# Optimization experiments

Measured on AMD Instinct MI355X. Metric: run time of the kernel, lower is better.

## Reference

```python
import jax, jax.numpy as jnp
import numpy as np

N_NODES = 50000
N_EDGES = 800000
IN_CH, HID_CH, OUT_CH = 128, 128, 64


def setup_inputs() -> dict:
    key = jax.random.key(0)
    k1, k2, k3, k4 = jax.random.split(key, 4)
    x = jax.random.normal(k1, (N_NODES, IN_CH), dtype=jnp.float32)
    edge_index = jax.random.randint(k2, (2, N_EDGES), 0, N_NODES, dtype=jnp.int64)
    W1 = jax.random.normal(k3, (IN_CH, HID_CH), dtype=jnp.float32) * (1.0 / np.sqrt(IN_CH))
    b1 = jnp.zeros((HID_CH,), dtype=jnp.float32)
    W2 = jax.random.normal(k4, (HID_CH, OUT_CH), dtype=jnp.float32) * (1.0 / np.sqrt(HID_CH))
    b2 = jnp.zeros((OUT_CH,), dtype=jnp.float32)
    return {"x": x, "edge_index": edge_index, "W1": W1, "b1": b1, "W2": W2, "b2": b2}


def _gcn_conv(x, src, dst, norm, W, b, n_nodes):
    # x' = D^-1/2 (A+I) D^-1/2 (x W) + b
    h = x @ W                                        # [N, C_out]
    msg = norm[:, None] * h[src]                     # gather + scale, [E', C_out]
    agg = jax.ops.segment_sum(msg, dst, num_segments=n_nodes)
    return agg + b


def reference(x, edge_index, W1, b1, W2, b2):
    n = x.shape[0]
    # add self loops
    loops = jnp.arange(n, dtype=edge_index.dtype)
    src = jnp.concatenate([edge_index[0], loops])
    dst = jnp.concatenate([edge_index[1], loops])
    # symmetric degree normalization computed on target index
    deg = jax.ops.segment_sum(jnp.ones_like(dst, dtype=x.dtype), dst, num_segments=n)
    dinv = jnp.where(deg > 0, jax.lax.rsqrt(deg), 0.0)
    norm = dinv[src] * dinv[dst]                     # [E']

    h = jax.nn.relu(_gcn_conv(x, src, dst, norm, W1, b1, n))
    logits = _gcn_conv(h, src, dst, norm, W2, b2, n)
    return jax.nn.softmax(logits, axis=1)
```

## Files before the change

kernel.cpp:

```cpp
#include <hip/hip_runtime.h>
#include <hip/hip_fp16.h>


#define SLOT 64
#define NB   49
#define CAP  18432
#define EPB  4096

__global__ __launch_bounds__(256) void k_part(const int* __restrict__ ei,
                                              int* __restrict__ bcur,
                                              unsigned int* __restrict__ bkt,
                                              int e) {
    __shared__ int sSrc[EPB];
    __shared__ int sDst[EPB];
    __shared__ int sCnt[64];
    int b0 = blockIdx.x * EPB;
    int cnt = min(EPB, e - b0);
    for (int i = threadIdx.x; i < cnt; i += 256) {
        sSrc[i] = ei[b0 + i];
        sDst[i] = ei[e + b0 + i];
    }
    if (threadIdx.x < 64) sCnt[threadIdx.x] = 0;
    __syncthreads();
    for (int i = threadIdx.x; i < cnt; i += 256)
        atomicAdd(&sCnt[sDst[i] >> 10], 1);
    __syncthreads();
    if (threadIdx.x < 64) {
        int c = sCnt[threadIdx.x];
        int gbase = (c > 0 && threadIdx.x < NB) ? atomicAdd(&bcur[threadIdx.x], c) : 0;
        sCnt[threadIdx.x] = gbase;
    }
    __syncthreads();
    for (int i = threadIdx.x; i < cnt; i += 256) {
        int d = sDst[i];
        int b = d >> 10;
        int pos = atomicAdd(&sCnt[b], 1);
        if (pos < CAP)
            bkt[(size_t)b * CAP + pos] =
                ((unsigned int)(d & 1023) << 16) | (unsigned int)sSrc[i];
    }
}

__global__ __launch_bounds__(256) void k_build(const int* __restrict__ bcur,
                                               const unsigned int* __restrict__ bkt,
                                               unsigned short* __restrict__ csr,
                                               int* __restrict__ deg,
                                               float* __restrict__ dinv, int n) {
    __shared__ unsigned short rows[256 * SLOT];
    __shared__ int cur[256];
    int r = blockIdx.x;
    int b = r >> 2;
    int q = r & 3;
    cur[threadIdx.x] = 0;
    __syncthreads();
    int cnt = min(bcur[b], CAP);
    const unsigned int* bp = bkt + (size_t)b * CAP;
    for (int i = threadIdx.x; i < cnt; i += 256) {
        unsigned int p = bp[i];
        int dl = (int)(p >> 16);
        if ((dl >> 8) == q) {
            int node = dl & 255;
            int pos = atomicAdd(&cur[node], 1);
            if (pos < SLOT) rows[node * SLOT + pos] = (unsigned short)(p & 0xffff);
        }
    }
    __syncthreads();
    int base = r * 256;
    uint4* dst4 = (uint4*)(csr + (size_t)base * SLOT);
    const uint4* src4 = (const uint4*)rows;
    for (int i = threadIdx.x; i < 256 * SLOT / 8; i += 256) dst4[i] = src4[i];
    int node = base + threadIdx.x;
    if (node < n) {
        int c = cur[threadIdx.x];
        deg[node] = c;
        dinv[node] = rsqrtf((float)(c + 1));
    }
}

__global__ __launch_bounds__(256, 4) void k_gemm1(
    const float* __restrict__ X, const float* __restrict__ W,
    __half* __restrict__ H, int n)
{
    __shared__ float sX[64 * 132];
    const int tid = threadIdx.x;
    const int r0 = blockIdx.x * 64;

    for (int i = tid; i < 64 * 32; i += 256) {
        int r = i >> 5, c4 = i & 31;
        float4 v = make_float4(0.f, 0.f, 0.f, 0.f);
        int gr = r0 + r;
        if (gr < n) v = ((const float4*)X)[(size_t)gr * 32 + c4];
        *(float4*)&sX[r * 132 + c4 * 4] = v;
    }
    __syncthreads();

    const int rg = tid >> 4;
    const int cg = tid & 15;
    float acc[4][8];
#pragma unroll
    for (int i = 0; i < 4; ++i)
#pragma unroll
        for (int j = 0; j < 8; ++j) acc[i][j] = 0.f;

    const float* sXr = sX + rg * 4 * 132;
    const float* Wc = W + cg * 8;
#pragma unroll 4
    for (int k = 0; k < 128; ++k) {
        float4 w0 = *(const float4*)(Wc + k * 128);
        float4 w1 = *(const float4*)(Wc + k * 128 + 4);
        float a[4];
#pragma unroll
        for (int i = 0; i < 4; ++i) a[i] = sXr[i * 132 + k];
        float w[8] = {w0.x, w0.y, w0.z, w0.w, w1.x, w1.y, w1.z, w1.w};
#pragma unroll
        for (int i = 0; i < 4; ++i)
#pragma unroll
            for (int j = 0; j < 8; ++j) acc[i][j] = fmaf(a[i], w[j], acc[i][j]);
    }

#pragma unroll
    for (int i = 0; i < 4; ++i) {
        int r = r0 + rg * 4 + i;
        if (r < n) {
            __half2 hp[4];
#pragma unroll
            for (int j = 0; j < 4; ++j)
                hp[j] = __floats2half2_rn(acc[i][2 * j], acc[i][2 * j + 1]);
            *(float4*)(H + (size_t)r * 128 + cg * 8) = *(float4*)hp;
        }
    }
}

__global__ __launch_bounds__(256) void k_agg1(
    const int* __restrict__ deg, const unsigned short* __restrict__ csr,
    const float* __restrict__ dinv, const __half* __restrict__ H,
    const float* __restrict__ b1, float* __restrict__ H1, int n)
{
    int node = blockIdx.x * 4 + (threadIdx.x >> 6);
    if (node >= n) return;
    int lane = threadIdx.x & 63;
    int g = lane >> 4, sub = lane & 15;
    float dd = dinv[node];

    float acc[8];
#pragma unroll
    for (int i = 0; i < 8; ++i) acc[i] = 0.f;

    int beg = node * SLOT;
    int cnt = min(deg[node], SLOT);
    {
        int m = cnt;
        int   s_l = (lane < m) ? (int)csr[beg + lane] : 0;
        float w_l = (lane < m) ? dinv[s_l] * dd : 0.f;
        int iters = (m + 3) >> 2;
#pragma unroll 4
        for (int t = 0; t < iters; ++t) {
            int j = 4 * t + g;
            int   s = __shfl(s_l, j);
            float w = __shfl(w_l, j);
            float4 raw = ((const float4*)(H + (size_t)s * 128))[sub];
            const __half2* h2 = (const __half2*)&raw;
#pragma unroll
            for (int q = 0; q < 4; ++q) {
                float2 v = __half22float2(h2[q]);
                acc[2 * q]     = fmaf(w, v.x, acc[2 * q]);
                acc[2 * q + 1] = fmaf(w, v.y, acc[2 * q + 1]);
            }
        }
    }
#pragma unroll
    for (int i = 0; i < 8; ++i) {
        acc[i] += __shfl_xor(acc[i], 16);
        acc[i] += __shfl_xor(acc[i], 32);
    }
    float4 sraw = ((const float4*)(H + (size_t)node * 128))[sub];
    const __half2* sh2 = (const __half2*)&sraw;
    float sl = dd * dd;
    float4 bb0 = ((const float4*)(b1 + sub * 8))[0];
    float4 bb1 = ((const float4*)(b1 + sub * 8))[1];
    float out[8];
#pragma unroll
    for (int q = 0; q < 4; ++q) {
        float2 v = __half22float2(sh2[q]);
        out[2 * q]     = fmaf(sl, v.x, acc[2 * q]);
        out[2 * q + 1] = fmaf(sl, v.y, acc[2 * q + 1]);
    }
    out[0] += bb0.x; out[1] += bb0.y; out[2] += bb0.z; out[3] += bb0.w;
    out[4] += bb1.x; out[5] += bb1.y; out[6] += bb1.z; out[7] += bb1.w;
#pragma unroll
    for (int i = 0; i < 8; ++i) out[i] = fmaxf(out[i], 0.f);
    float* op = H1 + (size_t)node * 128 + sub * 8;
    if (g == 0) *(float4*)op       = make_float4(out[0], out[1], out[2], out[3]);
    if (g == 1) *(float4*)(op + 4) = make_float4(out[4], out[5], out[6], out[7]);
}

__global__ __launch_bounds__(256, 4) void k_gemm2(
    const float* __restrict__ X, const float* __restrict__ W,
    __half* __restrict__ H2, int n)
{
    __shared__ float sX[64 * 132];
    const int tid = threadIdx.x;
    const int r0 = blockIdx.x * 64;

    for (int i = tid; i < 64 * 32; i += 256) {
        int r = i >> 5, c4 = i & 31;
        float4 v = make_float4(0.f, 0.f, 0.f, 0.f);
        int gr = r0 + r;
        if (gr < n) v = ((const float4*)X)[(size_t)gr * 32 + c4];
        *(float4*)&sX[r * 132 + c4 * 4] = v;
    }
    __syncthreads();

    const int rg = tid >> 4;
    const int cg = tid & 15;
    float acc[4][4];
#pragma unroll
    for (int i = 0; i < 4; ++i)
#pragma unroll
        for (int j = 0; j < 4; ++j) acc[i][j] = 0.f;

    const float* sXr = sX + rg * 4 * 132;
    const float* Wc = W + cg * 4;
#pragma unroll 4
    for (int k = 0; k < 128; ++k) {
        float4 w0 = *(const float4*)(Wc + k * 64);
        float a[4];
#pragma unroll
        for (int i = 0; i < 4; ++i) a[i] = sXr[i * 132 + k];
        float w[4] = {w0.x, w0.y, w0.z, w0.w};
#pragma unroll
        for (int i = 0; i < 4; ++i)
#pragma unroll
            for (int j = 0; j < 4; ++j) acc[i][j] = fmaf(a[i], w[j], acc[i][j]);
    }

#pragma unroll
    for (int i = 0; i < 4; ++i) {
        int r = r0 + rg * 4 + i;
        if (r < n) {
            __half2 hp[2];
            hp[0] = __floats2half2_rn(acc[i][0], acc[i][1]);
            hp[1] = __floats2half2_rn(acc[i][2], acc[i][3]);
            *(float2*)(H2 + (size_t)r * 64 + cg * 4) = *(float2*)hp;
        }
    }
}

__global__ __launch_bounds__(256) void k_agg2(
    const int* __restrict__ deg, const unsigned short* __restrict__ csr,
    const float* __restrict__ dinv, const __half* __restrict__ H2,
    const float* __restrict__ b2, float* __restrict__ OUT, int n)
{
    int node = blockIdx.x * 4 + (threadIdx.x >> 6);
    if (node >= n) return;
    int lane = threadIdx.x & 63;
    int g = lane >> 3, sub = lane & 7;
    float dd = dinv[node];

    float acc[8];
#pragma unroll
    for (int i = 0; i < 8; ++i) acc[i] = 0.f;

    int beg = node * SLOT;
    int cnt = min(deg[node], SLOT);
    {
        int m = cnt;
        int   s_l = (lane < m) ? (int)csr[beg + lane] : 0;
        float w_l = (lane < m) ? dinv[s_l] * dd : 0.f;
        int iters = (m + 7) >> 3;
#pragma unroll 4
        for (int t = 0; t < iters; ++t) {
            int j = 8 * t + g;
            int   s = __shfl(s_l, j);
            float w = __shfl(w_l, j);
            float4 raw = ((const float4*)(H2 + (size_t)s * 64))[sub];
            const __half2* h2 = (const __half2*)&raw;
#pragma unroll
            for (int q = 0; q < 4; ++q) {
                float2 v = __half22float2(h2[q]);
                acc[2 * q]     = fmaf(w, v.x, acc[2 * q]);
                acc[2 * q + 1] = fmaf(w, v.y, acc[2 * q + 1]);
            }
        }
    }
#pragma unroll
    for (int i = 0; i < 8; ++i) {
        acc[i] += __shfl_xor(acc[i], 8);
        acc[i] += __shfl_xor(acc[i], 16);
        acc[i] += __shfl_xor(acc[i], 32);
    }
    float4 sraw = ((const float4*)(H2 + (size_t)node * 64))[sub];
    const __half2* sh2 = (const __half2*)&sraw;
    float sl = dd * dd;
    float4 bb0 = ((const float4*)(b2 + sub * 8))[0];
    float4 bb1 = ((const float4*)(b2 + sub * 8))[1];
    float out[8];
#pragma unroll
    for (int q = 0; q < 4; ++q) {
        float2 v = __half22float2(sh2[q]);
        out[2 * q]     = fmaf(sl, v.x, acc[2 * q]);
        out[2 * q + 1] = fmaf(sl, v.y, acc[2 * q + 1]);
    }
    out[0] += bb0.x; out[1] += bb0.y; out[2] += bb0.z; out[3] += bb0.w;
    out[4] += bb1.x; out[5] += bb1.y; out[6] += bb1.z; out[7] += bb1.w;
    float mx = out[0];
#pragma unroll
    for (int i = 1; i < 8; ++i) mx = fmaxf(mx, out[i]);
    mx = fmaxf(mx, __shfl_xor(mx, 1));
    mx = fmaxf(mx, __shfl_xor(mx, 2));
    mx = fmaxf(mx, __shfl_xor(mx, 4));
    float sm = 0.f;
#pragma unroll
    for (int i = 0; i < 8; ++i) { out[i] = expf(out[i] - mx); sm += out[i]; }
    sm += __shfl_xor(sm, 1);
    sm += __shfl_xor(sm, 2);
    sm += __shfl_xor(sm, 4);
    float inv = 1.f / sm;
#pragma unroll
    for (int i = 0; i < 8; ++i) out[i] *= inv;
    float* op = OUT + (size_t)node * 64 + sub * 8;
    if (g == 0) *(float4*)op       = make_float4(out[0], out[1], out[2], out[3]);
    if (g == 1) *(float4*)(op + 4) = make_float4(out[4], out[5], out[6], out[7]);
}

extern "C" void kernel_launch(void* const* d_in, const int* in_sizes, int n_in,
                              void* d_out, int out_size, void* d_ws, size_t ws_size,
                              hipStream_t stream) {
    const float* X  = (const float*)d_in[0];
    const int*   EI = (const int*)d_in[1];
    const float* W1 = (const float*)d_in[2];
    const float* B1 = (const float*)d_in[3];
    const float* W2 = (const float*)d_in[4];
    const float* B2 = (const float*)d_in[5];
    float* OUT = (float*)d_out;

    const int n = in_sizes[0] / 128;
    const int e = in_sizes[1] / 2;

    const int np = (n + 255) & ~255;
    int*            bcur = (int*)d_ws;
    int*            deg  = bcur + 64;
    float*          dinv = (float*)(deg + np);
    unsigned int*   bkt  = (unsigned int*)(dinv + np);
    unsigned short* csr  = (unsigned short*)(bkt + (size_t)NB * CAP);
    __half*         H16  = (__half*)(csr + (size_t)np * SLOT);
    float*          H1   = (float*)(H16 + (size_t)np * 128);
    __half*         H2   = (__half*)(H1 + (size_t)n * 128);

    hipMemsetAsync(bcur, 0, 64 * sizeof(int), stream);
    k_part<<<(e + EPB - 1) / EPB, 256, 0, stream>>>(EI, bcur, bkt, e);
    k_build<<<np / 256, 256, 0, stream>>>(bcur, bkt, csr, deg, dinv, n);

    k_gemm1<<<(n + 63) / 64, 256, 0, stream>>>(X, W1, H16, n);
    k_agg1<<<(n + 3) / 4, 256, 0, stream>>>(deg, csr, dinv, H16, B1, H1, n);

    k_gemm2<<<(n + 63) / 64, 256, 0, stream>>>(H1, W2, H2, n);
    k_agg2<<<(n + 3) / 4, 256, 0, stream>>>(deg, csr, dinv, H2, B2, OUT, n);
}
```

Measured before the change: 241.4 us.

## Replace FP32 FMA GEMMs with split-fp16 MFMA matrix-core GEMMs

Both dense projections now run on MFMA 16x16x16 fp16 instructions instead of scalar FP32 FMAs through LDS. Each operand is split into hi and lo fp16 parts, and three MFMAs per tile keep accuracy close to FP32. A new kernel prepacks W1 and W2 into an MFMA-friendly split layout in the workspace. X is read straight from global memory with no shared-memory staging. The costs are one extra small launch and three MFMAs per tile, and the split-fp16 scheme can lose range for values outside fp16 limits.

```diff
diff --git a/kernel.cpp b/kernel.cpp
--- a/kernel.cpp
+++ b/kernel.cpp
@@ -6,6 +6,10 @@
 #define NB   49
 #define CAP  18432
 #define EPB  4096
+
+typedef _Float16 h4 __attribute__((ext_vector_type(4)));
+typedef _Float16 h8 __attribute__((ext_vector_type(8)));
+typedef float f4 __attribute__((ext_vector_type(4)));
 
 __global__ __launch_bounds__(256) void k_part(const int* __restrict__ ei,
                                               int* __restrict__ bcur,
@@ -77,56 +81,67 @@
     }
 }
 
-__global__ __launch_bounds__(256, 4) void k_gemm1(
-    const float* __restrict__ X, const float* __restrict__ W,
+__global__ __launch_bounds__(256) void k_splitw(const float* __restrict__ W1,
+                                                const float* __restrict__ W2,
+                                                _Float16* __restrict__ W1p,
+                                                _Float16* __restrict__ W2p) {
+    int i = blockIdx.x * 256 + threadIdx.x;
+    float w; int k, c; _Float16* dst;
+    if (i < 16384)      { k = i >> 7, c = i & 127; w = W1[i]; dst = W1p; }
+    else if (i < 24576) { int t = i - 16384; k = t >> 6; c = t & 63; w = W2[t]; dst = W2p; }
+    else return;
+    _Float16 hi = (_Float16)w;
+    _Float16 lo = (_Float16)(w - (float)hi);
+    int kc = k >> 4, kk = k & 15;
+    int l = (kk >> 2) * 16 + (c & 15);
+    int j = kk & 3;
+    int ct = c >> 4;
+    size_t base = ((size_t)(ct * 8 + kc) * 64 + l) * 8 + j;
+    dst[base] = hi;
+    dst[base + 4] = lo;
+}
+
+__global__ __launch_bounds__(256) void k_gemm1(
+    const float* __restrict__ X, const _Float16* __restrict__ Wp,
     __half* __restrict__ H, int n)
 {
-    __shared__ float sX[64 * 132];
-    const int tid = threadIdx.x;
-    const int r0 = blockIdx.x * 64;
-
-    for (int i = tid; i < 64 * 32; i += 256) {
-        int r = i >> 5, c4 = i & 31;
-        float4 v = make_float4(0.f, 0.f, 0.f, 0.f);
-        int gr = r0 + r;
-        if (gr < n) v = ((const float4*)X)[(size_t)gr * 32 + c4];
-        *(float4*)&sX[r * 132 + c4 * 4] = v;
-    }
-    __syncthreads();
-
-    const int rg = tid >> 4;
-    const int cg = tid & 15;
-    float acc[4][8];
-#pragma unroll
-    for (int i = 0; i < 4; ++i)
-#pragma unroll
-        for (int j = 0; j < 8; ++j) acc[i][j] = 0.f;
-
-    const float* sXr = sX + rg * 4 * 132;
-    const float* Wc = W + cg * 8;
-#pragma unroll 4
-    for (int k = 0; k < 128; ++k) {
-        float4 w0 = *(const float4*)(Wc + k * 128);
-        float4 w1 = *(const float4*)(Wc + k * 128 + 4);
-        float a[4];
-#pragma unroll
-        for (int i = 0; i < 4; ++i) a[i] = sXr[i * 132 + k];
-        float w[8] = {w0.x, w0.y, w0.z, w0.w, w1.x, w1.y, w1.z, w1.w};
-#pragma unroll
-        for (int i = 0; i < 4; ++i)
-#pragma unroll
-            for (int j = 0; j < 8; ++j) acc[i][j] = fmaf(a[i], w[j], acc[i][j]);
-    }
-
-#pragma unroll
-    for (int i = 0; i < 4; ++i) {
-        int r = r0 + rg * 4 + i;
-        if (r < n) {
-            __half2 hp[4];
-#pragma unroll
-            for (int j = 0; j < 4; ++j)
-                hp[j] = __floats2half2_rn(acc[i][2 * j], acc[i][2 * j + 1]);
-            *(float4*)(H + (size_t)r * 128 + cg * 8) = *(float4*)hp;
+    int w = threadIdx.x >> 6, lane = threadIdx.x & 63;
+    int r0 = blockIdx.x * 64 + w * 16;
+    int xr = r0 + (lane & 15);
+    int xrc = min(xr, n - 1);
+    const float* xp = X + (size_t)xrc * 128 + ((lane >> 4) * 4);
+
+    f4 acc[8];
+#pragma unroll
+    for (int ct = 0; ct < 8; ++ct) acc[ct] = (f4){0.f, 0.f, 0.f, 0.f};
+
+#pragma unroll
+    for (int kc = 0; kc < 8; ++kc) {
+        float4 xv = *(const float4*)(xp + kc * 16);
+        h4 xh, xl;
+        xh[0] = (_Float16)xv.x; xh[1] = (_Float16)xv.y;
+        xh[2] = (_Float16)xv.z; xh[3] = (_Float16)xv.w;
+        xl[0] = (_Float16)(xv.x - (float)xh[0]);
+        xl[1] = (_Float16)(xv.y - (float)xh[1]);
+        xl[2] = (_Float16)(xv.z - (float)xh[2]);
+        xl[3] = (_Float16)(xv.w - (float)xh[3]);
+#pragma unroll
+        for (int ct = 0; ct < 8; ++ct) {
+            h8 wb = ((const h8*)Wp)[(ct * 8 + kc) * 64 + lane];
+            h4 wh = {wb[0], wb[1], wb[2], wb[3]};
+            h4 wl = {wb[4], wb[5], wb[6], wb[7]};
+            acc[ct] = __builtin_amdgcn_mfma_f32_16x16x16f16(wh, xh, acc[ct], 0, 0, 0);
+            acc[ct] = __builtin_amdgcn_mfma_f32_16x16x16f16(wl, xh, acc[ct], 0, 0, 0);
+            acc[ct] = __builtin_amdgcn_mfma_f32_16x16x16f16(wh, xl, acc[ct], 0, 0, 0);
+        }
+    }
+    if (xr < n) {
+        __half* hp = H + (size_t)xr * 128 + (lane >> 4) * 4;
+#pragma unroll
+        for (int ct = 0; ct < 8; ++ct) {
+            h4 o = {(_Float16)acc[ct][0], (_Float16)acc[ct][1],
+                    (_Float16)acc[ct][2], (_Float16)acc[ct][3]};
+            *(h4*)(hp + ct * 16) = o;
         }
     }
 }
@@ -194,54 +209,47 @@
     if (g == 1) *(float4*)(op + 4) = make_float4(out[4], out[5], out[6], out[7]);
 }
 
-__global__ __launch_bounds__(256, 4) void k_gemm2(
-    const float* __restrict__ X, const float* __restrict__ W,
+__global__ __launch_bounds__(256) void k_gemm2(
+    const float* __restrict__ X, const _Float16* __restrict__ Wp,
     __half* __restrict__ H2, int n)
 {
-    __shared__ float sX[64 * 132];
-    const int tid = threadIdx.x;
-    const int r0 = blockIdx.x * 64;
-
-    for (int i = tid; i < 64 * 32; i += 256) {
-        int r = i >> 5, c4 = i & 31;
-        float4 v = make_float4(0.f, 0.f, 0.f, 0.f);
-        int gr = r0 + r;
-        if (gr < n) v = ((const float4*)X)[(size_t)gr * 32 + c4];
-        *(float4*)&sX[r * 132 + c4 * 4] = v;
-    }
-    __syncthreads();
-
-    const int rg = tid >> 4;
-    const int cg = tid & 15;
-    float acc[4][4];
-#pragma unroll
-    for (int i = 0; i < 4; ++i)
-#pragma unroll
-        for (int j = 0; j < 4; ++j) acc[i][j] = 0.f;
-
-    const float* sXr = sX + rg * 4 * 132;
-    const float* Wc = W + cg * 4;
-#pragma unroll 4
-    for (int k = 0; k < 128; ++k) {
-        float4 w0 = *(const float4*)(Wc + k * 64);
-        float a[4];
-#pragma unroll
-        for (int i = 0; i < 4; ++i) a[i] = sXr[i * 132 + k];
-        float w[4] = {w0.x, w0.y, w0.z, w0.w};
-#pragma unroll
-        for (int i = 0; i < 4; ++i)
-#pragma unroll
-            for (int j = 0; j < 4; ++j) acc[i][j] = fmaf(a[i], w[j], acc[i][j]);
-    }
-
-#pragma unroll
-    for (int i = 0; i < 4; ++i) {
-        int r = r0 + rg * 4 + i;
-        if (r < n) {
-            __half2 hp[2];
-            hp[0] = __floats2half2_rn(acc[i][0], acc[i][1]);
-            hp[1] = __floats2half2_rn(acc[i][2], acc[i][3]);
-            *(float2*)(H2 + (size_t)r * 64 + cg * 4) = *(float2*)hp;
+    int w = threadIdx.x >> 6, lane = threadIdx.x & 63;
+    int r0 = blockIdx.x * 64 + w * 16;
+    int xr = r0 + (lane & 15);
+    int xrc = min(xr, n - 1);
+    const float* xp = X + (size_t)xrc * 128 + ((lane >> 4) * 4);
+
+    f4 acc[4];
+#pragma unroll
+    for (int ct = 0; ct < 4; ++ct) acc[ct] = (f4){0.f, 0.f, 0.f, 0.f};
+
+#pragma unroll
+    for (int kc = 0; kc < 8; ++kc) {
+        float4 xv = *(const float4*)(xp + kc * 16);
+        h4 xh, xl;
+        xh[0] = (_Float16)xv.x; xh[1] = (_Float16)xv.y;
+        xh[2] = (_Float16)xv.z; xh[3] = (_Float16)xv.w;
+        xl[0] = (_Float16)(xv.x - (float)xh[0]);
+        xl[1] = (_Float16)(xv.y - (float)xh[1]);
+        xl[2] = (_Float16)(xv.z - (float)xh[2]);
+        xl[3] = (_Float16)(xv.w - (float)xh[3]);
+#pragma unroll
+        for (int ct = 0; ct < 4; ++ct) {
+            h8 wb = ((const h8*)Wp)[(ct * 8 + kc) * 64 + lane];
+            h4 wh = {wb[0], wb[1], wb[2], wb[3]};
+            h4 wl = {wb[4], wb[5], wb[6], wb[7]};
+            acc[ct] = __builtin_amdgcn_mfma_f32_16x16x16f16(wh, xh, acc[ct], 0, 0, 0);
+            acc[ct] = __builtin_amdgcn_mfma_f32_16x16x16f16(wl, xh, acc[ct], 0, 0, 0);
+            acc[ct] = __builtin_amdgcn_mfma_f32_16x16x16f16(wh, xl, acc[ct], 0, 0, 0);
+        }
+    }
+    if (xr < n) {
+        __half* hp = H2 + (size_t)xr * 64 + (lane >> 4) * 4;
+#pragma unroll
+        for (int ct = 0; ct < 4; ++ct) {
+            h4 o = {(_Float16)acc[ct][0], (_Float16)acc[ct][1],
+                    (_Float16)acc[ct][2], (_Float16)acc[ct][3]};
+            *(h4*)(hp + ct * 16) = o;
         }
     }
 }
@@ -343,17 +351,20 @@
     float*          dinv = (float*)(deg + np);
     unsigned int*   bkt  = (unsigned int*)(dinv + np);
     unsigned short* csr  = (unsigned short*)(bkt + (size_t)NB * CAP);
-    __half*         H16  = (__half*)(csr + (size_t)np * SLOT);
+    _Float16*       W1p  = (_Float16*)(csr + (size_t)np * SLOT);
+    _Float16*       W2p  = W1p + 32768;
+    __half*         H16  = (__half*)(W2p + 16384);
     float*          H1   = (float*)(H16 + (size_t)np * 128);
     __half*         H2   = (__half*)(H1 + (size_t)n * 128);
 
-    hipMemsetAsync(bcur, 0, 64 * sizeof(int), stream);
+    (void)hipMemsetAsync(bcur, 0, 64 * sizeof(int), stream);
+    k_splitw<<<96, 256, 0, stream>>>(W1, W2, W1p, W2p);
     k_part<<<(e + EPB - 1) / EPB, 256, 0, stream>>>(EI, bcur, bkt, e);
     k_build<<<np / 256, 256, 0, stream>>>(bcur, bkt, csr, deg, dinv, n);
 
-    k_gemm1<<<(n + 63) / 64, 256, 0, stream>>>(X, W1, H16, n);
+    k_gemm1<<<(n + 63) / 64, 256, 0, stream>>>(X, W1p, H16, n);
     k_agg1<<<(n + 3) / 4, 256, 0, stream>>>(deg, csr, dinv, H16, B1, H1, n);
 
-    k_gemm2<<<(n + 63) / 64, 256, 0, stream>>>(H1, W2, H2, n);
+    k_gemm2<<<(n + 63) / 64, 256, 0, stream>>>(H1, W2p, H2, n);
     k_agg2<<<(n + 3) / 4, 256, 0, stream>>>(deg, csr, dinv, H2, B2, OUT, n);
 }
```

Result: faster. 220.8 us (-8.5%).
